# Performance work log

Hardware: AMD Instinct MI355X
Metric: run time of the kernel (lower is better)

## Reference

```python
import jax, jax.numpy as jnp
import numpy as np

INPUT_DIM = 32
HID_DIM = 64
TTCN_DIM = HID_DIM - 1  # 63
N, LX = 128, 512


def setup_inputs() -> dict:
    key = jax.random.key(0)
    ks = jax.random.split(key, 10)
    X_int = jax.random.normal(ks[0], (N, LX, INPUT_DIM), dtype=jnp.float32)
    mask_X = jax.random.randint(ks[1], (N, LX, 1), 0, 2).astype(jnp.float32)
    s1 = 1.0 / np.sqrt(INPUT_DIM)
    s2 = 1.0 / np.sqrt(TTCN_DIM)
    W1 = jax.random.uniform(ks[2], (INPUT_DIM, TTCN_DIM), jnp.float32, -s1, s1)
    b1 = jax.random.uniform(ks[3], (TTCN_DIM,), jnp.float32, -s1, s1)
    W2 = jax.random.uniform(ks[4], (TTCN_DIM, TTCN_DIM), jnp.float32, -s2, s2)
    b2 = jax.random.uniform(ks[5], (TTCN_DIM,), jnp.float32, -s2, s2)
    W3 = jax.random.uniform(ks[6], (TTCN_DIM, INPUT_DIM * TTCN_DIM), jnp.float32, -s2, s2)
    b3 = jax.random.uniform(ks[7], (INPUT_DIM * TTCN_DIM,), jnp.float32, -s2, s2)
    T_bias = jax.random.normal(ks[8], (1, TTCN_DIM), dtype=jnp.float32)
    return {"X_int": X_int, "mask_X": mask_X, "W1": W1, "b1": b1,
            "W2": W2, "b2": b2, "W3": W3, "b3": b3, "T_bias": T_bias}


def reference(X_int, mask_X, W1, b1, W2, b2, W3, b3, T_bias):
    n, lx, d = X_int.shape
    k = TTCN_DIM
    # 3-layer MLP filter generator: (N, Lx, D*K)
    h = jax.nn.relu(X_int @ W1 + b1)
    h = jax.nn.relu(h @ W2 + b2)
    filt = h @ W3 + b3
    # masked softmax over the time axis Lx
    filt = filt * mask_X + (1.0 - mask_X) * (-1e8)
    filt = jax.nn.softmax(filt, axis=1)  # softmax over Lx
    filt = filt.reshape(n, lx, k, d)     # (N, Lx, K, D)
    # attention-weighted pooling: sum over Lx and D
    out = jnp.einsum('nld,nlkd->nk', X_int, filt)
    return jax.nn.relu(out + T_bias)
```

## Files before the change

kernel.cpp:

```cpp
#include <hip/hip_runtime.h>
#include <hip/hip_bf16.h>


#define N_   128
#define LX_  512
#define D_   32
#define K_   63
#define C_   2016

typedef __bf16 bf16x8 __attribute__((ext_vector_type(8)));
typedef float floatx4 __attribute__((ext_vector_type(4)));

static __device__ __forceinline__ floatx4 mfma16(bf16x8 a, bf16x8 b, floatx4 c) {
  return __builtin_amdgcn_mfma_f32_16x16x32_bf16(a, b, c, 0, 0, 0);
}

#define H_OFF    0u
#define W3FR_OFF (8u * 1024u * 1024u)
#define W1FR_OFF (W3FR_OFF + 258048u)
#define W2FR_OFF (W1FR_OFF + 4096u)
#define B1_OFF   (W2FR_OFF + 8192u)

__global__ __launch_bounds__(256) void kern_prep(
    const float* __restrict__ W1, const float* __restrict__ b1,
    const float* __restrict__ W2, const float* __restrict__ b2,
    const float* __restrict__ W3, const float* __restrict__ b3,
    __bf16* __restrict__ W3fr, __bf16* __restrict__ W1fr,
    __bf16* __restrict__ W2fr, float* __restrict__ b1pad) {
  const int g = blockIdx.x * 256 + threadIdx.x;
  if (g < 129024) {
    const int j = g & 7, quad = (g >> 3) & 3, l16 = (g >> 5) & 15, h = (g >> 9) & 1;
    const int rest = g >> 10, i = rest % 6, tile = rest / 6;
    const int c = tile * 96 + i * 16 + l16;
    const int t = h * 32 + quad * 8 + j;
    W3fr[g] = (__bf16)((t < K_) ? W3[(size_t)t * C_ + c] : b3[c]);
  } else if (g < 129024 + 2048) {
    const int g2 = g - 129024;
    const int j = g2 & 7, quad = (g2 >> 3) & 3, l16 = (g2 >> 5) & 15, i = g2 >> 9;
    const int ch = i * 16 + l16, t = quad * 8 + j;
    W1fr[g2] = (__bf16)((ch < K_) ? W1[t * K_ + ch] : 0.f);
  } else if (g < 129024 + 2048 + 4096) {
    const int g2 = g - 129024 - 2048;
    const int j = g2 & 7, quad = (g2 >> 3) & 3, l16 = (g2 >> 5) & 15, h = (g2 >> 9) & 1;
    const int i = g2 >> 10;
    const int ch = i * 16 + l16, t = h * 32 + quad * 8 + j;
    float v;
    if (t < K_) v = (ch < K_) ? W2[t * K_ + ch] : 0.f;
    else        v = (ch < K_) ? b2[ch] : 1.f;
    W2fr[g2] = (__bf16)v;
  } else if (g < 129024 + 2048 + 4096 + 64) {
    const int g2 = g - 129024 - 2048 - 4096;
    b1pad[g2] = (g2 < K_) ? b1[g2] : 0.f;
  }
}

__global__ __launch_bounds__(256) void kern_mlp(
    const float* __restrict__ X, const __bf16* __restrict__ W1fr,
    const __bf16* __restrict__ W2fr, const float* __restrict__ b1pad,
    __bf16* __restrict__ H) {
  __shared__ float h1s[4][16][68];
  const int tid = threadIdx.x;
  const int w = tid >> 6, lane = tid & 63, quad = lane >> 4, l16 = lane & 15;

  bf16x8 b1f[4], b2f[4][2];
  float b1v[4];
#pragma unroll
  for (int i = 0; i < 4; ++i) {
    b1f[i]    = *(const bf16x8*)(W1fr + ((i * 16 + l16) * 4 + quad) * 8);
    b2f[i][0] = *(const bf16x8*)(W2fr + (((i * 2 + 0) * 16 + l16) * 4 + quad) * 8);
    b2f[i][1] = *(const bf16x8*)(W2fr + (((i * 2 + 1) * 16 + l16) * 4 + quad) * 8);
    b1v[i] = b1pad[i * 16 + l16];
  }

  const int tok0 = blockIdx.x * 64 + w * 16;
  const float* xp = X + (size_t)(tok0 + l16) * D_ + quad * 8;
  const float4 xa = *(const float4*)xp;
  const float4 xb = *(const float4*)(xp + 4);
  bf16x8 a1;
  a1[0]=(__bf16)xa.x; a1[1]=(__bf16)xa.y; a1[2]=(__bf16)xa.z; a1[3]=(__bf16)xa.w;
  a1[4]=(__bf16)xb.x; a1[5]=(__bf16)xb.y; a1[6]=(__bf16)xb.z; a1[7]=(__bf16)xb.w;

#pragma unroll
  for (int i = 0; i < 4; ++i) {
    floatx4 acc = {0.f, 0.f, 0.f, 0.f};
    acc = mfma16(a1, b1f[i], acc);
#pragma unroll
    for (int r = 0; r < 4; ++r) {
      float v = fmaxf(acc[r] + b1v[i], 0.f);
      if (i == 3 && l16 == 15) v = 1.f;
      h1s[w][quad * 4 + r][i * 16 + l16] = v;
    }
  }
  __syncthreads();

  const float* hrow = &h1s[w][l16][0];
  const float4 p0 = *(const float4*)(hrow + quad * 8);
  const float4 p1 = *(const float4*)(hrow + quad * 8 + 4);
  const float4 p2 = *(const float4*)(hrow + 32 + quad * 8);
  const float4 p3 = *(const float4*)(hrow + 32 + quad * 8 + 4);
  bf16x8 a20, a21;
  a20[0]=(__bf16)p0.x; a20[1]=(__bf16)p0.y; a20[2]=(__bf16)p0.z; a20[3]=(__bf16)p0.w;
  a20[4]=(__bf16)p1.x; a20[5]=(__bf16)p1.y; a20[6]=(__bf16)p1.z; a20[7]=(__bf16)p1.w;
  a21[0]=(__bf16)p2.x; a21[1]=(__bf16)p2.y; a21[2]=(__bf16)p2.z; a21[3]=(__bf16)p2.w;
  a21[4]=(__bf16)p3.x; a21[5]=(__bf16)p3.y; a21[6]=(__bf16)p3.z; a21[7]=(__bf16)p3.w;

#pragma unroll
  for (int i = 0; i < 4; ++i) {
    floatx4 acc = {0.f, 0.f, 0.f, 0.f};
    acc = mfma16(a20, b2f[i][0], acc);
    acc = mfma16(a21, b2f[i][1], acc);
#pragma unroll
    for (int r = 0; r < 4; ++r)
      H[(size_t)(tok0 + quad * 4 + r) * 64 + i * 16 + l16] =
          (__bf16)fmaxf(acc[r], 0.f);
  }
}

__global__ __launch_bounds__(256) void kern_att(
    const float* __restrict__ X, const float* __restrict__ Mk,
    const __bf16* __restrict__ H, const __bf16* __restrict__ W3fr,
    const float* __restrict__ Tb, float* __restrict__ out) {
  __shared__ float redS[4][96], redO[4][96];
  __shared__ float rbuf[96];

  const int bid = blockIdx.x;
  const int idx = bid >> 3;
  const int n = (bid & 7) * 16 + idx / 21;
  const int bt = idx % 21;
  const int tid = threadIdx.x;
  const int w = tid >> 6, lane = tid & 63, quad = lane >> 4, l16 = lane & 15;

  bf16x8 bf[6][2];
#pragma unroll
  for (int i = 0; i < 6; ++i) {
    bf[i][0] = *(const bf16x8*)(W3fr + ((((bt * 6 + i) * 2 + 0) * 16 + l16) * 4 + quad) * 8);
    bf[i][1] = *(const bf16x8*)(W3fr + ((((bt * 6 + i) * 2 + 1) * 16 + l16) * 4 + quad) * 8);
  }

  float s[6] = {0, 0, 0, 0, 0, 0}, o[6] = {0, 0, 0, 0, 0, 0};

#pragma unroll 1
  for (int it = 0; it < 8; ++it) {
    const int lw = it * 64 + w * 16;
    const __bf16* hp = H + (size_t)(n * LX_ + lw + l16) * 64;
    const bf16x8 a0 = *(const bf16x8*)(hp + quad * 8);
    const bf16x8 a1 = *(const bf16x8*)(hp + 32 + quad * 8);
    const float4 mk4 = *(const float4*)(Mk + n * LX_ + lw + quad * 4);
    const float* xrow = X + (size_t)(n * LX_ + lw + quad * 4) * D_;
    float xlo[4], xhi[4];
#pragma unroll
    for (int r = 0; r < 4; ++r) {
      xlo[r] = xrow[r * D_ + l16];
      xhi[r] = xrow[r * D_ + 16 + l16];
    }

#pragma unroll
    for (int i = 0; i < 6; ++i) {
      floatx4 acc = {0.f, 0.f, 0.f, 0.f};
      acc = mfma16(a0, bf[i][0], acc);
      acc = mfma16(a1, bf[i][1], acc);
      const float* xv = (i & 1) ? xhi : xlo;
      const float e0 = __expf(acc[0]) * mk4.x;
      const float e1 = __expf(acc[1]) * mk4.y;
      const float e2 = __expf(acc[2]) * mk4.z;
      const float e3 = __expf(acc[3]) * mk4.w;
      s[i] += (e0 + e1) + (e2 + e3);
      o[i] = fmaf(e0, xv[0], o[i]);
      o[i] = fmaf(e1, xv[1], o[i]);
      o[i] = fmaf(e2, xv[2], o[i]);
      o[i] = fmaf(e3, xv[3], o[i]);
    }
  }

#pragma unroll
  for (int i = 0; i < 6; ++i) {
    s[i] += __shfl_xor(s[i], 16);
    s[i] += __shfl_xor(s[i], 32);
    o[i] += __shfl_xor(o[i], 16);
    o[i] += __shfl_xor(o[i], 32);
  }
  if (quad == 0) {
#pragma unroll
    for (int i = 0; i < 6; ++i) {
      redS[w][i * 16 + l16] = s[i];
      redO[w][i * 16 + l16] = o[i];
    }
  }
  __syncthreads();
  if (tid < 96) {
    const float S = redS[0][tid] + redS[1][tid] + redS[2][tid] + redS[3][tid];
    const float O = redO[0][tid] + redO[1][tid] + redO[2][tid] + redO[3][tid];
    rbuf[tid] = O / S;
  }
  __syncthreads();
  if (tid < 3) {
    float acc = 0.f;
#pragma unroll
    for (int dd = 0; dd < 32; ++dd) acc += rbuf[tid * 32 + dd];
    const int k = bt * 3 + tid;
    out[n * K_ + k] = fmaxf(acc + Tb[k], 0.f);
  }
}

extern "C" void kernel_launch(void* const* d_in, const int* in_sizes, int n_in,
                              void* d_out, int out_size, void* d_ws, size_t ws_size,
                              hipStream_t stream) {
  const float* X  = (const float*)d_in[0];
  const float* Mk = (const float*)d_in[1];
  const float* W1 = (const float*)d_in[2];
  const float* b1 = (const float*)d_in[3];
  const float* W2 = (const float*)d_in[4];
  const float* b2 = (const float*)d_in[5];
  const float* W3 = (const float*)d_in[6];
  const float* b3 = (const float*)d_in[7];
  const float* Tb = (const float*)d_in[8];
  float* out = (float*)d_out;

  char* ws = (char*)d_ws;
  __bf16* H     = (__bf16*)(ws + H_OFF);
  __bf16* W3fr  = (__bf16*)(ws + W3FR_OFF);
  __bf16* W1fr  = (__bf16*)(ws + W1FR_OFF);
  __bf16* W2fr  = (__bf16*)(ws + W2FR_OFF);
  float*  b1pad = (float*)(ws + B1_OFF);

  kern_prep<<<529, 256, 0, stream>>>(W1, b1, W2, b2, W3, b3, W3fr, W1fr, W2fr, b1pad);
  kern_mlp<<<N_ * LX_ / 64, 256, 0, stream>>>(X, W1fr, W2fr, b1pad, H);
  kern_att<<<N_ * 21, 256, 0, stream>>>(X, Mk, H, W3fr, Tb, out);
}
```

Before: 128.8 us.

## Compact masked-out timesteps so attention kernel only processes valid tokens

The prep kernel now builds per-batch prefix positions and counts from the mask via wave ballots. The MLP kernel scatters H and a bf16 copy of X only for unmasked tokens into compacted buffers. The attention kernel then iterates only over ceil(count/64) chunks, which should remove roughly half the MFMA/exp work given the random binary mask. It also folds log2e into W3 to use exp2 directly and adds register double-buffering of the next chunk's loads. The costs are extra prep work and a serialized scan, and X now enters the weighted sum in bf16 rather than fp32. Removing the __syncthreads in the MLP kernel relies on each wave reading only its own h1s rows.

```diff
diff --git a/kernel.cpp b/kernel.cpp
--- a/kernel.cpp
+++ b/kernel.cpp
@@ -7,6 +7,7 @@
 #define D_   32
 #define K_   63
 #define C_   2016
+#define LOG2E 1.44269504088896f
 
 typedef __bf16 bf16x8 __attribute__((ext_vector_type(8)));
 typedef float floatx4 __attribute__((ext_vector_type(4)));
@@ -15,49 +16,83 @@
   return __builtin_amdgcn_mfma_f32_16x16x32_bf16(a, b, c, 0, 0, 0);
 }
 
-#define H_OFF    0u
-#define W3FR_OFF (8u * 1024u * 1024u)
+#define HC_OFF   0u
+#define XMC_OFF  (8u * 1024u * 1024u)
+#define W3FR_OFF (12u * 1024u * 1024u)
 #define W1FR_OFF (W3FR_OFF + 258048u)
 #define W2FR_OFF (W1FR_OFF + 4096u)
 #define B1_OFF   (W2FR_OFF + 8192u)
+#define POS_OFF  (B1_OFF + 256u)
+#define CNT_OFF  (POS_OFF + 262144u)
 
 __global__ __launch_bounds__(256) void kern_prep(
+    const float* __restrict__ Mk,
     const float* __restrict__ W1, const float* __restrict__ b1,
     const float* __restrict__ W2, const float* __restrict__ b2,
     const float* __restrict__ W3, const float* __restrict__ b3,
     __bf16* __restrict__ W3fr, __bf16* __restrict__ W1fr,
-    __bf16* __restrict__ W2fr, float* __restrict__ b1pad) {
-  const int g = blockIdx.x * 256 + threadIdx.x;
-  if (g < 129024) {
-    const int j = g & 7, quad = (g >> 3) & 3, l16 = (g >> 5) & 15, h = (g >> 9) & 1;
-    const int rest = g >> 10, i = rest % 6, tile = rest / 6;
-    const int c = tile * 96 + i * 16 + l16;
-    const int t = h * 32 + quad * 8 + j;
-    W3fr[g] = (__bf16)((t < K_) ? W3[(size_t)t * C_ + c] : b3[c]);
-  } else if (g < 129024 + 2048) {
-    const int g2 = g - 129024;
-    const int j = g2 & 7, quad = (g2 >> 3) & 3, l16 = (g2 >> 5) & 15, i = g2 >> 9;
-    const int ch = i * 16 + l16, t = quad * 8 + j;
-    W1fr[g2] = (__bf16)((ch < K_) ? W1[t * K_ + ch] : 0.f);
-  } else if (g < 129024 + 2048 + 4096) {
-    const int g2 = g - 129024 - 2048;
-    const int j = g2 & 7, quad = (g2 >> 3) & 3, l16 = (g2 >> 5) & 15, h = (g2 >> 9) & 1;
-    const int i = g2 >> 10;
-    const int ch = i * 16 + l16, t = h * 32 + quad * 8 + j;
-    float v;
-    if (t < K_) v = (ch < K_) ? W2[t * K_ + ch] : 0.f;
-    else        v = (ch < K_) ? b2[ch] : 1.f;
-    W2fr[g2] = (__bf16)v;
-  } else if (g < 129024 + 2048 + 4096 + 64) {
-    const int g2 = g - 129024 - 2048 - 4096;
-    b1pad[g2] = (g2 < K_) ? b1[g2] : 0.f;
+    __bf16* __restrict__ W2fr, float* __restrict__ b1pad,
+    int* __restrict__ pos, int* __restrict__ cnt,
+    __bf16* __restrict__ Hc, __bf16* __restrict__ Xmc) {
+  const int n = blockIdx.x, tid = threadIdx.x;
+  __shared__ int s_cnt;
+
+  if (tid < 64) {
+    const int lane = tid;
+    int running = 0;
+    for (int c = 0; c < 8; ++c) {
+      const int l = c * 64 + lane;
+      const float mkv = Mk[n * LX_ + l];
+      const unsigned long long b = __ballot(mkv > 0.5f);
+      const int mypos = running + __popcll(b & ((1ull << lane) - 1ull));
+      pos[n * LX_ + l] = (mkv > 0.5f) ? mypos : -1;
+      running += __popcll(b);
+    }
+    if (lane == 0) { cnt[n] = running; s_cnt = running; }
+  }
+  __syncthreads();
+
+  const int c0 = s_cnt, c1 = (c0 + 63) & ~63;
+  const float4 z = {0.f, 0.f, 0.f, 0.f};
+  for (int idx = tid; idx < (c1 - c0) * 12; idx += 256) {
+    const int row = c0 + idx / 12, q = idx % 12;
+    if (q < 8) *(float4*)(Hc  + ((size_t)(n * 512 + row)) * 64 + q * 8) = z;
+    else       *(float4*)(Xmc + ((size_t)(n * 512 + row)) * 32 + (q - 8) * 8) = z;
+  }
+
+  for (int g = n * 256 + tid; g < 129024 + 2048 + 4096 + 64; g += N_ * 256) {
+    if (g < 129024) {
+      const int j = g & 7, quad = (g >> 3) & 3, l16 = (g >> 5) & 15, h = (g >> 9) & 1;
+      const int rest = g >> 10, i = rest % 6, tile = rest / 6;
+      const int c = tile * 96 + i * 16 + l16;
+      const int t = h * 32 + quad * 8 + j;
+      W3fr[g] = (__bf16)(((t < K_) ? W3[(size_t)t * C_ + c] : b3[c]) * LOG2E);
+    } else if (g < 129024 + 2048) {
+      const int g2 = g - 129024;
+      const int j = g2 & 7, quad = (g2 >> 3) & 3, l16 = (g2 >> 5) & 15, i = g2 >> 9;
+      const int ch = i * 16 + l16, t = quad * 8 + j;
+      W1fr[g2] = (__bf16)((ch < K_) ? W1[t * K_ + ch] : 0.f);
+    } else if (g < 129024 + 2048 + 4096) {
+      const int g2 = g - 129024 - 2048;
+      const int j = g2 & 7, quad = (g2 >> 3) & 3, l16 = (g2 >> 5) & 15, h = (g2 >> 9) & 1;
+      const int i = g2 >> 10;
+      const int ch = i * 16 + l16, t = h * 32 + quad * 8 + j;
+      float v;
+      if (t < K_) v = (ch < K_) ? W2[t * K_ + ch] : 0.f;
+      else        v = (ch < K_) ? b2[ch] : 1.f;
+      W2fr[g2] = (__bf16)v;
+    } else {
+      const int g2 = g - 129024 - 2048 - 4096;
+      b1pad[g2] = (g2 < K_) ? b1[g2] : 0.f;
+    }
   }
 }
 
 __global__ __launch_bounds__(256) void kern_mlp(
     const float* __restrict__ X, const __bf16* __restrict__ W1fr,
     const __bf16* __restrict__ W2fr, const float* __restrict__ b1pad,
-    __bf16* __restrict__ H) {
+    const int* __restrict__ pos, __bf16* __restrict__ Hc,
+    __bf16* __restrict__ Xmc) {
   __shared__ float h1s[4][16][68];
   const int tid = threadIdx.x;
   const int w = tid >> 6, lane = tid & 63, quad = lane >> 4, l16 = lane & 15;
@@ -73,6 +108,7 @@
   }
 
   const int tok0 = blockIdx.x * 64 + w * 16;
+  const int n = tok0 >> 9;
   const float* xp = X + (size_t)(tok0 + l16) * D_ + quad * 8;
   const float4 xa = *(const float4*)xp;
   const float4 xb = *(const float4*)(xp + 4);
@@ -80,6 +116,14 @@
   a1[0]=(__bf16)xa.x; a1[1]=(__bf16)xa.y; a1[2]=(__bf16)xa.z; a1[3]=(__bf16)xa.w;
   a1[4]=(__bf16)xb.x; a1[5]=(__bf16)xb.y; a1[6]=(__bf16)xb.z; a1[7]=(__bf16)xb.w;
 
+  const int px = pos[tok0 + l16];
+  int pr[4];
+#pragma unroll
+  for (int r = 0; r < 4; ++r) pr[r] = pos[tok0 + quad * 4 + r];
+
+  if (px >= 0)
+    *(bf16x8*)(Xmc + ((size_t)(n * 512 + px)) * 32 + quad * 8) = a1;
+
 #pragma unroll
   for (int i = 0; i < 4; ++i) {
     floatx4 acc = {0.f, 0.f, 0.f, 0.f};
@@ -91,7 +135,6 @@
       h1s[w][quad * 4 + r][i * 16 + l16] = v;
     }
   }
-  __syncthreads();
 
   const float* hrow = &h1s[w][l16][0];
   const float4 p0 = *(const float4*)(hrow + quad * 8);
@@ -110,15 +153,17 @@
     acc = mfma16(a20, b2f[i][0], acc);
     acc = mfma16(a21, b2f[i][1], acc);
 #pragma unroll
-    for (int r = 0; r < 4; ++r)
-      H[(size_t)(tok0 + quad * 4 + r) * 64 + i * 16 + l16] =
-          (__bf16)fmaxf(acc[r], 0.f);
+    for (int r = 0; r < 4; ++r) {
+      if (pr[r] >= 0)
+        Hc[((size_t)(n * 512 + pr[r])) * 64 + i * 16 + l16] =
+            (__bf16)fmaxf(acc[r], 0.f);
+    }
   }
 }
 
 __global__ __launch_bounds__(256) void kern_att(
-    const float* __restrict__ X, const float* __restrict__ Mk,
-    const __bf16* __restrict__ H, const __bf16* __restrict__ W3fr,
+    const __bf16* __restrict__ Hc, const __bf16* __restrict__ Xmc,
+    const __bf16* __restrict__ W3fr, const int* __restrict__ cnt,
     const float* __restrict__ Tb, float* __restrict__ out) {
   __shared__ float redS[4][96], redO[4][96];
   __shared__ float rbuf[96];
@@ -137,39 +182,61 @@
     bf[i][1] = *(const bf16x8*)(W3fr + ((((bt * 6 + i) * 2 + 1) * 16 + l16) * 4 + quad) * 8);
   }
 
+  const int cntn = cnt[n];
+  const int iters = (cntn + 63) >> 6;
+  const __bf16* Hn = Hc + ((size_t)n << 9) * 64;
+  const __bf16* Xn = Xmc + ((size_t)n << 9) * 32;
+
   float s[6] = {0, 0, 0, 0, 0, 0}, o[6] = {0, 0, 0, 0, 0, 0};
 
+  int lw = w * 16;
+  bf16x8 a0 = *(const bf16x8*)(Hn + (size_t)(lw + l16) * 64 + quad * 8);
+  bf16x8 a1 = *(const bf16x8*)(Hn + (size_t)(lw + l16) * 64 + 32 + quad * 8);
+  float xl[4], xh[4];
+#pragma unroll
+  for (int r = 0; r < 4; ++r) {
+    xl[r] = (float)Xn[(lw + quad * 4 + r) * 32 + l16];
+    xh[r] = (float)Xn[(lw + quad * 4 + r) * 32 + 16 + l16];
+  }
+
 #pragma unroll 1
-  for (int it = 0; it < 8; ++it) {
-    const int lw = it * 64 + w * 16;
-    const __bf16* hp = H + (size_t)(n * LX_ + lw + l16) * 64;
-    const bf16x8 a0 = *(const bf16x8*)(hp + quad * 8);
-    const bf16x8 a1 = *(const bf16x8*)(hp + 32 + quad * 8);
-    const float4 mk4 = *(const float4*)(Mk + n * LX_ + lw + quad * 4);
-    const float* xrow = X + (size_t)(n * LX_ + lw + quad * 4) * D_;
-    float xlo[4], xhi[4];
-#pragma unroll
-    for (int r = 0; r < 4; ++r) {
-      xlo[r] = xrow[r * D_ + l16];
-      xhi[r] = xrow[r * D_ + 16 + l16];
-    }
+  for (int it = 0;;) {
+    bf16x8 na0, na1;
+    float nxl[4], nxh[4];
+    const int nlw = lw + 64;
+    if (it + 1 < iters) {
+      na0 = *(const bf16x8*)(Hn + (size_t)(nlw + l16) * 64 + quad * 8);
+      na1 = *(const bf16x8*)(Hn + (size_t)(nlw + l16) * 64 + 32 + quad * 8);
+#pragma unroll
+      for (int r = 0; r < 4; ++r) {
+        nxl[r] = (float)Xn[(nlw + quad * 4 + r) * 32 + l16];
+        nxh[r] = (float)Xn[(nlw + quad * 4 + r) * 32 + 16 + l16];
+      }
+    }
+
+    float v[4];
+#pragma unroll
+    for (int r = 0; r < 4; ++r) v[r] = (lw + quad * 4 + r < cntn) ? 1.f : 0.f;
 
 #pragma unroll
     for (int i = 0; i < 6; ++i) {
       floatx4 acc = {0.f, 0.f, 0.f, 0.f};
       acc = mfma16(a0, bf[i][0], acc);
       acc = mfma16(a1, bf[i][1], acc);
-      const float* xv = (i & 1) ? xhi : xlo;
-      const float e0 = __expf(acc[0]) * mk4.x;
-      const float e1 = __expf(acc[1]) * mk4.y;
-      const float e2 = __expf(acc[2]) * mk4.z;
-      const float e3 = __expf(acc[3]) * mk4.w;
-      s[i] += (e0 + e1) + (e2 + e3);
-      o[i] = fmaf(e0, xv[0], o[i]);
-      o[i] = fmaf(e1, xv[1], o[i]);
-      o[i] = fmaf(e2, xv[2], o[i]);
-      o[i] = fmaf(e3, xv[3], o[i]);
-    }
+      const float* xv = (i & 1) ? xh : xl;
+#pragma unroll
+      for (int r = 0; r < 4; ++r) {
+        const float e = __builtin_amdgcn_exp2f(acc[r]);
+        s[i] = fmaf(v[r], e, s[i]);
+        o[i] = fmaf(e, xv[r], o[i]);
+      }
+    }
+
+    if (++it >= iters) break;
+    lw = nlw;
+    a0 = na0; a1 = na1;
+#pragma unroll
+    for (int r = 0; r < 4; ++r) { xl[r] = nxl[r]; xh[r] = nxh[r]; }
   }
 
 #pragma unroll
@@ -217,13 +284,17 @@
   float* out = (float*)d_out;
 
   char* ws = (char*)d_ws;
-  __bf16* H     = (__bf16*)(ws + H_OFF);
+  __bf16* Hc    = (__bf16*)(ws + HC_OFF);
+  __bf16* Xmc   = (__bf16*)(ws + XMC_OFF);
   __bf16* W3fr  = (__bf16*)(ws + W3FR_OFF);
   __bf16* W1fr  = (__bf16*)(ws + W1FR_OFF);
   __bf16* W2fr  = (__bf16*)(ws + W2FR_OFF);
   float*  b1pad = (float*)(ws + B1_OFF);
-
-  kern_prep<<<529, 256, 0, stream>>>(W1, b1, W2, b2, W3, b3, W3fr, W1fr, W2fr, b1pad);
-  kern_mlp<<<N_ * LX_ / 64, 256, 0, stream>>>(X, W1fr, W2fr, b1pad, H);
-  kern_att<<<N_ * 21, 256, 0, stream>>>(X, Mk, H, W3fr, Tb, out);
-}
+  int*    pos   = (int*)(ws + POS_OFF);
+  int*    cnt   = (int*)(ws + CNT_OFF);
+
+  kern_prep<<<N_, 256, 0, stream>>>(Mk, W1, b1, W2, b2, W3, b3,
+                                    W3fr, W1fr, W2fr, b1pad, pos, cnt, Hc, Xmc);
+  kern_mlp<<<N_ * LX_ / 64, 256, 0, stream>>>(X, W1fr, W2fr, b1pad, pos, Hc, Xmc);
+  kern_att<<<N_ * 21, 256, 0, stream>>>(Hc, Xmc, W3fr, cnt, Tb, out);
+}
```

Result: faster. 113.7 us (-11.7%).
